# Kernel tuning notes

Hardware: AMD Instinct MI355X
Metric: run time of the kernel (lower is better)

## Reference

```python
import jax, jax.numpy as jnp
import numpy as np

N_NODE = 50000   # item vocab
D = 100          # embed_dim / hidden_size
N = 49152        # total nodes across all sessions
E = 98304        # edges
B = 4096         # sessions
STDV = 1.0 / np.sqrt(D)


def setup_inputs() -> dict:
    key = jax.random.key(0)
    ks = jax.random.split(key, 20)
    # 1-based item ids, shape [N,1] as in data.x
    x = jax.random.randint(ks[0], (N, 1), 1, N_NODE + 1, dtype=jnp.int32)
    edge_index = jax.random.randint(ks[1], (2, E), 0, N, dtype=jnp.int32)
    # sorted session ids; every session appears at least once (split/nodes[-1] needs non-empty)
    base = jnp.arange(B, dtype=jnp.int32)
    extra = jax.random.randint(ks[2], (N - B,), 0, B, dtype=jnp.int32)
    batch = jnp.sort(jnp.concatenate([base, extra]))

    def u(k, shape):
        return jax.random.uniform(k, shape, minval=-STDV, maxval=STDV, dtype=jnp.float32)

    return {
        "x": x, "edge_index": edge_index, "batch": batch, "num_sessions": B,
        "emb": u(ks[3], (N_NODE, D)),
        "conv_w": u(ks[4], (D, D)),          # GatedGraphConv weight[0]
        "gru_w_ih": u(ks[5], (3 * D, D)),
        "gru_w_hh": u(ks[6], (3 * D, D)),
        "gru_b_ih": u(ks[7], (3 * D,)),
        "gru_b_hh": u(ks[8], (3 * D,)),
        "q_w": u(ks[9], (1, D)), "q_b": u(ks[10], (1,)),
        "w2_w": u(ks[11], (D, D)), "w2_b": u(ks[12], (D,)),
        "w3_w": u(ks[13], (D, D)), "w3_b": u(ks[14], (D,)),
        "w4_w": u(ks[15], (D, 3 * D)), "w4_b": u(ks[16], (D,)),
    }


def _forward(x, edge_index, batch, num_sessions, emb, conv_w,
             gru_w_ih, gru_w_hh, gru_b_ih, gru_b_hh,
             q_w, q_b, w2_w, w2_b, w3_w, w3_b, w4_w, w4_b):
    ids = x[:, 0] - 1                              # data.x - 1
    h0 = emb[ids]                                  # [N, D]

    # GatedGraphConv(num_layers=1): m = x @ W; aggregate sum src->dst; GRUCell update
    src, dst = edge_index[0], edge_index[1]
    m = h0 @ conv_w                                # [N, D]
    agg = jnp.zeros_like(h0).at[dst].add(m[src])   # segment-sum aggregation
    gi = agg @ gru_w_ih.T + gru_b_ih               # [N, 3D]
    gh = h0 @ gru_w_hh.T + gru_b_hh
    i_r, i_z, i_n = jnp.split(gi, 3, axis=1)
    h_r, h_z, h_n = jnp.split(gh, 3, axis=1)
    r = jax.nn.sigmoid(i_r + h_r)
    z = jax.nn.sigmoid(i_z + h_z)
    n = jnp.tanh(i_n + r * h_n)
    xh = jax.nn.relu((1.0 - z) * n + z * h0)       # F.relu(Conv(x, edge_index))

    # last node per session (batch is sorted, sessions non-empty)
    counts = jax.ops.segment_sum(jnp.ones_like(batch), batch, num_segments=num_sessions)
    last_idx = jnp.cumsum(counts) - 1
    v_n = xh[last_idx]                             # [B, D]

    # get_scores: per-session softmax(v_n . nodes) weighted sum -> S_s
    logits = jnp.sum(xh * v_n[batch], axis=1)      # [N]
    mx = jax.ops.segment_max(logits, batch, num_segments=num_sessions)
    p = jnp.exp(logits - mx[batch])
    denom = jax.ops.segment_sum(p, batch, num_segments=num_sessions)
    score = p / denom[batch]                       # [N]
    S_s = jax.ops.segment_sum(score[:, None] * xh, batch, num_segments=num_sessions)

    # sigmoid-gated attention pooling -> S_g
    gate = jax.nn.sigmoid(xh @ w2_w.T + w2_b + v_n[batch] @ w3_w.T + w3_b)
    alpha = gate @ q_w.T + q_b                     # [N, 1]
    S_g = jax.ops.segment_sum(alpha * xh, batch, num_segments=num_sessions)

    S = jnp.concatenate([S_s, S_g, v_n], axis=1) @ w4_w.T + w4_b  # [B, D]
    y_hat = S @ emb.T                              # [B, n_node]
    return y_hat


def reference(x, edge_index, batch, num_sessions, emb, conv_w,
              gru_w_ih, gru_w_hh, gru_b_ih, gru_b_hh,
              q_w, q_b, w2_w, w2_b, w3_w, w3_b, w4_w, w4_b):
    return _forward(x, edge_index, batch, num_sessions, emb, conv_w,
                    gru_w_ih, gru_w_hh, gru_b_ih, gru_b_hh,
                    q_w, q_b, w2_w, w2_b, w3_w, w3_b, w4_w, w4_b)
```

## Files before the change

kernel.cpp:

```cpp
#include <hip/hip_runtime.h>
#include <math.h>

#define DDIM 100
#define PFD  4
#define NTG  4

using short8 = __attribute__((ext_vector_type(8))) short;
using f32x4  = __attribute__((ext_vector_type(4))) float;


__device__ __forceinline__ float sigm(float x) { return 1.f / (1.f + expf(-x)); }

__device__ __forceinline__ f32x4 mfma16(short8 a, short8 b, f32x4 c) {
  return __builtin_amdgcn_mfma_f32_16x16x32_bf16(a, b, c, 0, 0, 0);
}

__device__ __forceinline__ void gld_lds16(const void* g, void* l) {
  __builtin_amdgcn_global_load_lds(
      (const __attribute__((address_space(1))) void*)g,
      (__attribute__((address_space(3))) void*)l, 16, 0, 0);
}

__device__ __forceinline__ void bf16split(float v, short& h, short& l) {
  unsigned u = __float_as_uint(v);
  unsigned hb = (u + 0x7fffu + ((u >> 16) & 1u)) & 0xffff0000u;
  float res = v - __uint_as_float(hb);
  unsigned u2 = __float_as_uint(res);
  h = (short)(hb >> 16);
  l = (short)((u2 + 0x7fffu + ((u2 >> 16) & 1u)) >> 16);
}

__device__ __forceinline__ short bf16hi(float v) {
  unsigned u = __float_as_uint(v);
  return (short)((u + 0x7fffu + ((u >> 16) & 1u)) >> 16);
}

__global__ __launch_bounds__(256) void k_wc(const float* __restrict__ w_ih,
                                            const float* __restrict__ conv_w,
                                            float* __restrict__ Wc) {
  __shared__ float cwT[100 * 100];
  const int tid = threadIdx.x;
  for (int idx = tid; idx < 10000; idx += 256) {
    int k = idx / 100, t = idx - k * 100;
    cwT[t * 100 + k] = conv_w[idx];
  }
  __syncthreads();
  const int cBase = blockIdx.x * 25;
  for (int o = tid; o < 25 * 100; o += 256) {
    int c = cBase + o / 100;
    int k = o - (o / 100) * 100;
    const float* wr = w_ih + (size_t)c * 100;
    float acc = 0.f;
    for (int t = 0; t < 100; ++t) acc = fmaf(wr[t], cwT[t * 100 + k], acc);
    Wc[(size_t)c * 100 + k] = acc;
  }
}

__global__ void k_packAll(const int* __restrict__ batch, const float* __restrict__ emb,
                          const float* __restrict__ Wc,
                          const float* __restrict__ w_hh, const float* __restrict__ w2,
                          const float* __restrict__ w3,
                          short8* __restrict__ Bhi, short8* __restrict__ Blo,
                          short8* __restrict__ Whi, int* __restrict__ last_idx,
                          int NNODE, int NT, int N) {
  int gid = blockIdx.x * 256 + threadIdx.x;
  const int embN = NT * 4 * 64;
  const int wN = 8 * 7 * 4 * 64;
  if (gid < embN) {
    int lane = gid & 63;
    int kt = (gid >> 6) & 3;
    int rt = gid >> 8;
    int r = rt * 16 + (lane & 15);
    if (r >= NNODE) r = NNODE - 1;
    int k0 = kt * 32 + (lane >> 4) * 8;
    float4 f0 = make_float4(0.f, 0.f, 0.f, 0.f);
    float4 f1 = make_float4(0.f, 0.f, 0.f, 0.f);
    if (k0 < 100)     f0 = *(const float4*)(emb + (size_t)r * DDIM + k0);
    if (k0 + 4 < 100) f1 = *(const float4*)(emb + (size_t)r * DDIM + k0 + 4);
    float v[8] = {f0.x, f0.y, f0.z, f0.w, f1.x, f1.y, f1.z, f1.w};
    short8 h, l;
#pragma unroll
    for (int j = 0; j < 8; ++j) {
      short hh, ll;
      bf16split(v[j], hh, ll);
      h[j] = hh; l[j] = ll;
    }
    Bhi[gid] = h;
    Blo[gid] = l;
  } else if (gid < embN + wN) {
    int wg = gid - embN;
    int lane = wg & 63;
    int kt = (wg >> 6) & 3;
    int snt = wg >> 8;
    int nt = snt % 7;
    int s = snt / 7;
    int d = nt * 16 + (lane & 15);
    int k0 = kt * 32 + (lane >> 4) * 8;
    short8 h;
#pragma unroll
    for (int j = 0; j < 8; ++j) {
      int k = k0 + j;
      float v = 0.f;
      if (d < 100 && k < 100) {
        if (s < 3)      v = Wc[(size_t)(s * 100 + d) * 100 + k];
        else if (s < 6) v = w_hh[(size_t)((s - 3) * 100 + d) * 100 + k];
        else if (s == 6) v = w2[(size_t)d * 100 + k];
        else             v = w3[(size_t)d * 100 + k];
      }
      h[j] = bf16hi(v);
    }
    Whi[wg] = h;
  } else {
    int i = gid - embN - wN;
    if (i < N) {
      if (i == N - 1 || batch[i + 1] != batch[i]) last_idx[batch[i]] = i;
    }
  }
}

__global__ __launch_bounds__(512, 1) void k_aggGru(
    const int* __restrict__ ei, const int* __restrict__ x,
    const float* __restrict__ emb, const short8* __restrict__ Whi,
    const float* __restrict__ b_ih, const float* __restrict__ b_hh,
    const float* __restrict__ b2,
    float* __restrict__ xh, float* __restrict__ t2, int E) {
  __shared__ float acc[256 * DDIM];
  const int tid = threadIdx.x;
  const int lane = tid & 63;
  const int wave = tid >> 6;
  const int r0blk = blockIdx.x * 256;

  for (int idx = tid; idx < 256 * DDIM / 4; idx += 512)
    ((float4*)acc)[idx] = make_float4(0.f, 0.f, 0.f, 0.f);
  __syncthreads();

  const int per = E >> 3;
  const int base = wave * per;
  for (int it = 0; it < per; it += 256) {
    int e0 = base + it + lane * 4;
    int4 d4 = *(const int4*)(ei + E + e0);
    int4 s4 = *(const int4*)(ei + e0);
    int darr[4] = {d4.x, d4.y, d4.z, d4.w};
    int sarr[4] = {s4.x, s4.y, s4.z, s4.w};
#pragma unroll
    for (int j = 0; j < 4; ++j) {
      int dj = darr[j] - r0blk;
      bool match = (unsigned)dj < 256u;
      unsigned long long mask = __ballot(match);
      while (mask) {
        int bit = __ffsll(mask) - 1;
        mask &= mask - 1;
        int ds = __shfl(dj, bit, 64);
        int ss = __shfl(sarr[j], bit, 64);
        if (lane < 25) {
          int er = x[ss] - 1;
          float4 v = *(const float4*)(emb + (size_t)er * DDIM + 4 * lane);
          float* a = acc + ds * DDIM + 4 * lane;
          atomicAdd(a + 0, v.x); atomicAdd(a + 1, v.y);
          atomicAdd(a + 2, v.z); atomicAdd(a + 3, v.w);
        }
      }
    }
  }
  __syncthreads();

  const int lr = wave * 32;
  const int rowBase = r0blk + lr;
  const int c0 = lane & 15;
  const int rq = (lane >> 4) * 4;

  short8 aI0[4], aI1[4];
  {
    int r = lane & 15;
    int g = lane >> 4;
#pragma unroll
    for (int kt = 0; kt < 4; ++kt) {
      int k0 = kt * 32 + g * 8;
      short8 h0f, h1f;
#pragma unroll
      for (int j = 0; j < 8; ++j) {
        int k = k0 + j;
        float v0 = (k < 100) ? acc[(lr + r) * DDIM + k] : 0.f;
        float v1 = (k < 100) ? acc[(lr + 16 + r) * DDIM + k] : 0.f;
        h0f[j] = bf16hi(v0);
        h1f[j] = bf16hi(v1);
      }
      aI0[kt] = h0f;
      aI1[kt] = h1f;
    }
  }
  short8 aH0[4], aH1[4];
  {
    int r0g = x[rowBase + (lane & 15)] - 1;
    int r1g = x[rowBase + 16 + (lane & 15)] - 1;
    int g = lane >> 4;
#pragma unroll
    for (int kt = 0; kt < 4; ++kt) {
      int k0 = kt * 32 + g * 8;
      float4 a0f = make_float4(0.f, 0.f, 0.f, 0.f), a1f = a0f;
      float4 b0f = a0f, b1f = a0f;
      if (k0 < 100) {
        a0f = *(const float4*)(emb + (size_t)r0g * DDIM + k0);
        b0f = *(const float4*)(emb + (size_t)r1g * DDIM + k0);
      }
      if (k0 + 4 < 100) {
        a1f = *(const float4*)(emb + (size_t)r0g * DDIM + k0 + 4);
        b1f = *(const float4*)(emb + (size_t)r1g * DDIM + k0 + 4);
      }
      float v0[8] = {a0f.x, a0f.y, a0f.z, a0f.w, a1f.x, a1f.y, a1f.z, a1f.w};
      float v1[8] = {b0f.x, b0f.y, b0f.z, b0f.w, b1f.x, b1f.y, b1f.z, b1f.w};
      short8 h0f, h1f;
#pragma unroll
      for (int j = 0; j < 8; ++j) {
        h0f[j] = bf16hi(v0[j]);
        h1f[j] = bf16hi(v1[j]);
      }
      aH0[kt] = h0f;
      aH1[kt] = h1f;
    }
  }
  int xr0[4], xr1[4];
#pragma unroll
  for (int ri = 0; ri < 4; ++ri) {
    xr0[ri] = x[rowBase + rq + ri] - 1;
    xr1[ri] = x[rowBase + 16 + rq + ri] - 1;
  }

  for (int nt = 0; nt < 7; ++nt) {
    int d = nt * 16 + c0;
    f32x4 a0[6] = {};
    f32x4 a1[6] = {};
#pragma unroll
    for (int s = 0; s < 6; ++s) {
#pragma unroll
      for (int kt = 0; kt < 4; ++kt) {
        short8 w = Whi[(((size_t)s * 7 + nt) * 4 + kt) * 64 + lane];
        if (s < 3) {
          a0[s] = mfma16(aI0[kt], w, a0[s]);
          a1[s] = mfma16(aI1[kt], w, a1[s]);
        } else {
          a0[s] = mfma16(aH0[kt], w, a0[s]);
          a1[s] = mfma16(aH1[kt], w, a1[s]);
        }
      }
    }
    if (d < 100) {
      float bir = b_ih[d], biz = b_ih[100 + d], bin_ = b_ih[200 + d];
      float bhr = b_hh[d], bhz = b_hh[100 + d], bhn = b_hh[200 + d];
#pragma unroll
      for (int ri = 0; ri < 4; ++ri) {
        {
          float r = sigm(a0[0][ri] + bir + a0[3][ri] + bhr);
          float z = sigm(a0[1][ri] + biz + a0[4][ri] + bhz);
          float n = tanhf(a0[2][ri] + bin_ + r * (a0[5][ri] + bhn));
          float h0v = emb[(size_t)xr0[ri] * DDIM + d];
          float v = (1.f - z) * n + z * h0v;
          acc[(lr + rq + ri) * DDIM + d] = v > 0.f ? v : 0.f;
        }
        {
          float r = sigm(a1[0][ri] + bir + a1[3][ri] + bhr);
          float z = sigm(a1[1][ri] + biz + a1[4][ri] + bhz);
          float n = tanhf(a1[2][ri] + bin_ + r * (a1[5][ri] + bhn));
          float h0v = emb[(size_t)xr1[ri] * DDIM + d];
          float v = (1.f - z) * n + z * h0v;
          acc[(lr + 16 + rq + ri) * DDIM + d] = v > 0.f ? v : 0.f;
        }
      }
    }
  }

  const int dr = lane / 25;
  const int dc4 = (lane - dr * 25) * 4;
  if (lane < 50) {
#pragma unroll
    for (int p = 0; p < 16; ++p) {
      int row = p * 2 + dr;
      f32x4 v = *(const f32x4*)&acc[(lr + row) * DDIM + dc4];
      *(f32x4*)(xh + (size_t)(rowBase + row) * DDIM + dc4) = v;
    }
  }

  short8 xa0[4], xa1[4];
  {
    int r = lane & 15;
    int g = lane >> 4;
#pragma unroll
    for (int kt = 0; kt < 4; ++kt) {
      int k0 = kt * 32 + g * 8;
      short8 h0f, h1f;
#pragma unroll
      for (int j = 0; j < 8; ++j) {
        int k = k0 + j;
        float v0 = (k < 100) ? acc[(lr + r) * DDIM + k] : 0.f;
        float v1 = (k < 100) ? acc[(lr + 16 + r) * DDIM + k] : 0.f;
        h0f[j] = bf16hi(v0);
        h1f[j] = bf16hi(v1);
      }
      xa0[kt] = h0f;
      xa1[kt] = h1f;
    }
  }

  for (int nt = 0; nt < 7; ++nt) {
    int d = nt * 16 + c0;
    f32x4 ac0 = {0.f, 0.f, 0.f, 0.f};
    f32x4 ac1 = {0.f, 0.f, 0.f, 0.f};
#pragma unroll
    for (int kt = 0; kt < 4; ++kt) {
      short8 w = Whi[(((size_t)6 * 7 + nt) * 4 + kt) * 64 + lane];
      ac0 = mfma16(xa0[kt], w, ac0);
      ac1 = mfma16(xa1[kt], w, ac1);
    }
    if (d < 100) {
      float b = b2[d];
#pragma unroll
      for (int ri = 0; ri < 4; ++ri) {
        acc[(lr + rq + ri) * DDIM + d] = ac0[ri] + b;
        acc[(lr + 16 + rq + ri) * DDIM + d] = ac1[ri] + b;
      }
    }
  }
  if (lane < 50) {
#pragma unroll
    for (int p = 0; p < 16; ++p) {
      int row = p * 2 + dr;
      f32x4 v = *(const f32x4*)&acc[(lr + row) * DDIM + dc4];
      *(f32x4*)(t2 + (size_t)(rowBase + row) * DDIM + dc4) = v;
    }
  }
}

__global__ __launch_bounds__(256) void k_session(
    const float* __restrict__ xh, const float* __restrict__ t2,
    const float* __restrict__ t3v,
    const float* __restrict__ q_w, const float* __restrict__ q_b,
    const int* __restrict__ last_idx, float* __restrict__ Scat, int B) {
  int sid = blockIdx.x * 4 + (threadIdx.x >> 6);
  if (sid >= B) return;
  const int lane = threadIdx.x & 63;
  const int g = lane >> 4;
  const int s = lane & 15;
  const int start = (sid == 0) ? 0 : last_idx[sid - 1] + 1;
  const int end = last_idx[sid];

  float vr[7], t3r[7], qr[7];
#pragma unroll
  for (int k = 0; k < 7; ++k) {
    int c = s + 16 * k;
    bool ok = c < DDIM;
    vr[k]  = ok ? xh[(size_t)end * DDIM + c] : 0.f;
    t3r[k] = ok ? t3v[(size_t)sid * DDIM + c] : 0.f;
    qr[k]  = ok ? q_w[c] : 0.f;
  }
  const float qb = q_b[0];

  float m = -INFINITY, den = 0.f;
  float ss[7] = {}, sg[7] = {};
  for (int i = start; i <= end; i += 4) {
    int ni = i + g;
    bool act = ni <= end;
    int nrow = act ? ni : end;
    float xv[7];
    float l = 0.f, ga = 0.f;
#pragma unroll
    for (int k = 0; k < 7; ++k) {
      int c = s + 16 * k;
      float x = (c < DDIM) ? xh[(size_t)nrow * DDIM + c] : 0.f;
      float tv = (c < DDIM) ? t2[(size_t)nrow * DDIM + c] : 0.f;
      xv[k] = x;
      l = fmaf(x, vr[k], l);
      ga = fmaf(qr[k], sigm(tv + t3r[k]), ga);
    }
#pragma unroll
    for (int o = 1; o <= 8; o <<= 1) {
      l += __shfl_xor(l, o, 64);
      ga += __shfl_xor(ga, o, 64);
    }
    float ls = act ? l : -INFINITY;
    float alpha = act ? (ga + qb) : 0.f;
    float mn = fmaxf(m, ls);
    float cf = (m == -INFINITY) ? 0.f : expf(m - mn);
    float p = act ? expf(ls - mn) : 0.f;
    den = den * cf + p;
#pragma unroll
    for (int k = 0; k < 7; ++k) {
      ss[k] = ss[k] * cf + p * xv[k];
      sg[k] = fmaf(alpha, xv[k], sg[k]);
    }
    m = mn;
  }
  float mAll = m;
  mAll = fmaxf(mAll, __shfl_xor(mAll, 16, 64));
  mAll = fmaxf(mAll, __shfl_xor(mAll, 32, 64));
  float sc = (m == -INFINITY) ? 0.f : expf(m - mAll);
  float dv = den * sc;
  dv += __shfl_xor(dv, 16, 64);
  dv += __shfl_xor(dv, 32, 64);
  float inv = 1.f / dv;
  float* Sc = Scat + (size_t)sid * 300;
#pragma unroll
  for (int k = 0; k < 7; ++k) {
    float sv = ss[k] * sc;
    float gv = sg[k];
    sv += __shfl_xor(sv, 16, 64);  sv += __shfl_xor(sv, 32, 64);
    gv += __shfl_xor(gv, 16, 64);  gv += __shfl_xor(gv, 32, 64);
    int c = s + 16 * k;
    if (g == 0 && c < DDIM) {
      Sc[c] = sv * inv;
      Sc[100 + c] = gv;
      Sc[200 + c] = vr[k];
    }
  }
}

__device__ __forceinline__ void load_afragsHg(const float* __restrict__ A,
                                              const int* __restrict__ idx, int base,
                                              int lane, short8 ah[4]) {
  int r = idx[base + (lane & 15)];
  int g = lane >> 4;
#pragma unroll
  for (int kt = 0; kt < 4; ++kt) {
    int k0 = kt * 32 + g * 8;
    float4 f0 = make_float4(0.f, 0.f, 0.f, 0.f);
    float4 f1 = make_float4(0.f, 0.f, 0.f, 0.f);
    if (k0 < 100)     f0 = *(const float4*)(A + (size_t)r * DDIM + k0);
    if (k0 + 4 < 100) f1 = *(const float4*)(A + (size_t)r * DDIM + k0 + 4);
    short8 h;
    h[0] = bf16hi(f0.x); h[1] = bf16hi(f0.y); h[2] = bf16hi(f0.z); h[3] = bf16hi(f0.w);
    h[4] = bf16hi(f1.x); h[5] = bf16hi(f1.y); h[6] = bf16hi(f1.z); h[7] = bf16hi(f1.w);
    ah[kt] = h;
  }
}

__global__ __launch_bounds__(256) void k_t3v(
    const float* __restrict__ xh, const short8* __restrict__ Whi,
    const float* __restrict__ b3, const int* __restrict__ lastI,
    float* __restrict__ t3v) {
  const int lane = threadIdx.x & 63;
  const int wave = threadIdx.x >> 6;
  const int rowBase = blockIdx.x * 128 + wave * 32;
  short8 a0[4], a1[4];
  load_afragsHg(xh, lastI, rowBase, lane, a0);
  load_afragsHg(xh, lastI, rowBase + 16, lane, a1);
  const int c0 = lane & 15;
  const int r0 = (lane >> 4) * 4;

  for (int nt = 0; nt < 7; ++nt) {
    int d = nt * 16 + c0;
    f32x4 ac0 = {0.f, 0.f, 0.f, 0.f};
    f32x4 ac1 = {0.f, 0.f, 0.f, 0.f};
#pragma unroll
    for (int kt = 0; kt < 4; ++kt) {
      short8 w = Whi[(((size_t)7 * 7 + nt) * 4 + kt) * 64 + lane];
      ac0 = mfma16(a0[kt], w, ac0);
      ac1 = mfma16(a1[kt], w, ac1);
    }
    if (d < 100) {
      float b = b3[d];
#pragma unroll
      for (int ri = 0; ri < 4; ++ri) {
        t3v[(size_t)(rowBase + r0 + ri) * DDIM + d] = ac0[ri] + b;
        t3v[(size_t)(rowBase + 16 + r0 + ri) * DDIM + d] = ac1[ri] + b;
      }
    }
  }
}

__global__ __launch_bounds__(256, 2) void k_gemmS(
    const float* __restrict__ A, const float* __restrict__ Bm,
    const float* __restrict__ bias, short* __restrict__ Ph, short* __restrict__ Pl,
    int M) {
  __shared__ float4 As4[25 * 128];
  __shared__ float4 Bs4[25 * 64];
  const int m0 = blockIdx.y * 128;
  const int n0 = blockIdx.x * 64;
  const int t = threadIdx.x;
  const int tx = t & 15;
  const int ty = t >> 4;
  float acc[8][4] = {};

  for (int kt = 0; kt < 300; kt += 100) {
    for (int idx = t; idx < 128 * 25; idx += 256) {
      int r = idx / 25, k4 = idx - r * 25;
      int ar = m0 + r; if (ar >= M) ar = M - 1;
      float4 v = *(const float4*)(A + (size_t)ar * 300 + kt + 4 * k4);
      As4[k4 * 128 + (r ^ (k4 & 7))] = v;
    }
    for (int idx = t; idx < 64 * 25; idx += 256) {
      int r = idx / 25, k4 = idx - r * 25;
      int br = n0 + r;
      float4 v = make_float4(0.f, 0.f, 0.f, 0.f);
      if (br < 100) v = *(const float4*)(Bm + (size_t)br * 300 + kt + 4 * k4);
      Bs4[k4 * 64 + (r ^ (k4 & 7))] = v;
    }
    __syncthreads();
#pragma unroll 5
    for (int k4 = 0; k4 < 25; ++k4) {
      const int s = k4 & 7;
      float4 av[8], bv[4];
#pragma unroll
      for (int i = 0; i < 8; ++i) av[i] = As4[k4 * 128 + ((ty + 16 * i) ^ s)];
#pragma unroll
      for (int j = 0; j < 4; ++j) bv[j] = Bs4[k4 * 64 + ((tx + 16 * j) ^ s)];
#pragma unroll
      for (int i = 0; i < 8; ++i) {
#pragma unroll
        for (int j = 0; j < 4; ++j) {
          acc[i][j] = fmaf(av[i].x, bv[j].x, acc[i][j]);
          acc[i][j] = fmaf(av[i].y, bv[j].y, acc[i][j]);
          acc[i][j] = fmaf(av[i].z, bv[j].z, acc[i][j]);
          acc[i][j] = fmaf(av[i].w, bv[j].w, acc[i][j]);
        }
      }
    }
    __syncthreads();
  }

#pragma unroll
  for (int i = 0; i < 8; ++i) {
    int row = m0 + ty + 16 * i;
    if (row >= M) continue;
#pragma unroll
    for (int j = 0; j < 4; ++j) {
      int col = n0 + tx + 16 * j;
      float v = (col < 100) ? (acc[i][j] + bias[col]) : 0.f;
      short hh, ll;
      bf16split(v, hh, ll);
      int rt = row >> 4, kt = col >> 5;
      int lane_t = (row & 15) + 16 * ((col >> 3) & 3);
      size_t base = ((((size_t)rt * 4 + kt) * 64 + lane_t) << 3) + (col & 7);
      Ph[base] = hh;
      Pl[base] = ll;
    }
  }
}

__global__ __launch_bounds__(256) void k_bigmm(
    const short8* __restrict__ Ahi, const short8* __restrict__ Alo,
    const short8* __restrict__ Bhi, const short8* __restrict__ Blo,
    float* __restrict__ out, int NT, int NTCHUNK, int NCOLS) {
  __shared__ short8 Bs[PFD * 8 * 64];
  __shared__ float Xp[4 * 32 * 64];
  const int lane = threadIdx.x & 63;
  const int wave = threadIdx.x >> 6;
  const int mt0 = blockIdx.x * 8 + wave * 2;

  short8 ah[2][4], al[2][4];
#pragma unroll
  for (int mi = 0; mi < 2; ++mi)
#pragma unroll
    for (int kt = 0; kt < 4; ++kt) {
      size_t off = ((size_t)(mt0 + mi) * 4 + kt) * 64 + lane;
      ah[mi][kt] = Ahi[off];
      al[mi][kt] = Alo[off];
    }

  const int nt0 = blockIdx.y * NTCHUNK;
  const int nt1 = min(NT, nt0 + NTCHUNK);
  const int r0 = (lane >> 4) * 4;
  const int c0 = lane & 15;
  float* xp = &Xp[wave * 32 * 64];

  auto issueB = [&](int nt) {
    int s = nt & (PFD - 1);
    gld_lds16(Bhi + ((size_t)nt * 4 + wave) * 64 + lane, &Bs[(s * 8 + wave) * 64]);
    gld_lds16(Blo + ((size_t)nt * 4 + wave) * 64 + lane, &Bs[(s * 8 + 4 + wave) * 64]);
  };

  for (int i = 0; i < PFD && nt0 + i < nt1; ++i) issueB(nt0 + i);
  asm volatile("s_waitcnt vmcnt(6)" ::: "memory");
  __builtin_amdgcn_s_barrier();

  for (int g = nt0; g < nt1; g += NTG) {
    const int jn = min(NTG, nt1 - g);
    f32x4 acc[2][NTG] = {};
#pragma unroll
    for (int j = 0; j < NTG; ++j) {
      if (j >= jn) break;
      const int nt = g + j;
      const int s = nt & (PFD - 1);
      short8 bh[4], bl[4];
#pragma unroll
      for (int kt = 0; kt < 4; ++kt) {
        bh[kt] = Bs[(s * 8 + kt) * 64 + lane];
        bl[kt] = Bs[(s * 8 + 4 + kt) * 64 + lane];
      }
      asm volatile("s_waitcnt lgkmcnt(0)" ::: "memory");
      __builtin_amdgcn_s_barrier();
      if (nt + PFD < nt1) issueB(nt + PFD);
      __builtin_amdgcn_sched_barrier(0);
#pragma unroll
      for (int kt = 0; kt < 4; ++kt) {
        acc[0][j] = mfma16(ah[0][kt], bh[kt], acc[0][j]);
        acc[1][j] = mfma16(ah[1][kt], bh[kt], acc[1][j]);
        acc[0][j] = mfma16(ah[0][kt], bl[kt], acc[0][j]);
        acc[1][j] = mfma16(ah[1][kt], bl[kt], acc[1][j]);
        acc[0][j] = mfma16(al[0][kt], bh[kt], acc[0][j]);
        acc[1][j] = mfma16(al[1][kt], bh[kt], acc[1][j]);
      }
      asm volatile("s_waitcnt vmcnt(14)" ::: "memory");
      __builtin_amdgcn_s_barrier();
    }
#pragma unroll
    for (int mi = 0; mi < 2; ++mi)
#pragma unroll
      for (int j = 0; j < NTG; ++j) {
        if (j < jn) {
#pragma unroll
          for (int r = 0; r < 4; ++r) {
            int rl = mi * 16 + r0 + r;
            int cl = j * 16 + c0;
            xp[rl * 64 + (cl ^ (((rl >> 2) & 3) << 4))] = acc[mi][j][r];
          }
        }
      }
    const int colbase = g * 16;
#pragma unroll
    for (int it = 0; it < 8; ++it) {
      int rl = it * 4 + (lane >> 4);
      int cl = 4 * c0;
      if (cl < jn * 16) {
        f32x4 v = *(const f32x4*)&xp[rl * 64 + (cl ^ (((rl >> 2) & 3) << 4))];
        int row = mt0 * 16 + rl;
        __builtin_nontemporal_store(v, (f32x4*)(out + (size_t)row * NCOLS + colbase + cl));
      }
    }
  }
}


extern "C" void kernel_launch(void* const* d_in, const int* in_sizes, int n_in,
                              void* d_out, int out_size, void* d_ws, size_t ws_size,
                              hipStream_t stream) {
  const int*   x      = (const int*)d_in[0];
  const int*   ei     = (const int*)d_in[1];
  const int*   batch  = (const int*)d_in[2];
  const float* emb    = (const float*)d_in[4];
  const float* conv_w = (const float*)d_in[5];
  const float* w_ih   = (const float*)d_in[6];
  const float* w_hh   = (const float*)d_in[7];
  const float* b_ih   = (const float*)d_in[8];
  const float* b_hh   = (const float*)d_in[9];
  const float* q_w    = (const float*)d_in[10];
  const float* q_b    = (const float*)d_in[11];
  const float* w2     = (const float*)d_in[12];
  const float* b2     = (const float*)d_in[13];
  const float* w3     = (const float*)d_in[14];
  const float* b3     = (const float*)d_in[15];
  const float* w4     = (const float*)d_in[16];
  const float* b4     = (const float*)d_in[17];

  const int N = in_sizes[0];
  const int E = in_sizes[1] / 2;
  const int NNODE = in_sizes[4] / DDIM;
  const int B = out_size / NNODE;

  size_t ND = (size_t)N * DDIM;
  float* ws   = (float*)d_ws;
  float* xh   = ws;
  float* t2   = ws + ND;
  float* aux  = ws + 2 * ND;
  float* t3v  = aux;
  float* Scat = t3v + (size_t)B * DDIM;
  int*   lastI = (int*)(Scat + 3 * (size_t)B * DDIM);

  const int MT = (B + 15) / 16;
  const int NT = (NNODE + 15) / 16;
  short8* Whi = (short8*)(lastI + B);
  short8* Ahi = Whi + 8 * 7 * 4 * 64;
  short8* Alo = Ahi + (size_t)MT * 4 * 64;
  short8* Bhi = Alo + (size_t)MT * 4 * 64;
  short8* Blo = Bhi + (size_t)NT * 4 * 64;
  float*  Wc  = (float*)(Blo + (size_t)NT * 4 * 64);

  dim3 blk(256);
  const int nblkB = B / 128;

  int packTotal = NT * 4 * 64 + 8 * 7 * 4 * 64 + N;
  k_wc<<<12, blk, 0, stream>>>(w_ih, conv_w, Wc);
  k_packAll<<<(packTotal + 255) / 256, blk, 0, stream>>>(
      batch, emb, Wc, w_hh, w2, w3, Bhi, Blo, Whi, lastI, NNODE, NT, N);
  k_aggGru<<<N / 256, dim3(512), 0, stream>>>(ei, x, emb, Whi, b_ih, b_hh, b2,
                                              xh, t2, E);
  k_t3v<<<nblkB, blk, 0, stream>>>(xh, Whi, b3, lastI, t3v);
  k_session<<<(B + 3) / 4, blk, 0, stream>>>(xh, t2, t3v, q_w, q_b, lastI, Scat, B);
  k_gemmS<<<dim3(2, B / 128), blk, 0, stream>>>(Scat, w4, b4, (short*)Ahi, (short*)Alo, B);

  const int NTCHUNK = 48;
  const int NCHUNKS = (NT + NTCHUNK - 1) / NTCHUNK;
  k_bigmm<<<dim3(nblkB, NCHUNKS), blk, 0, stream>>>(
      Ahi, Alo, Bhi, Blo, (float*)d_out, NT, NTCHUNK, NNODE);
}
```

Baseline: 394.2 us.

## Compact matching edges into LDS queue before per-thread row accumulation

Edge-scatter aggregation no longer uses a per-match ballot/shuffle loop where only 25 lanes of a wave gather one embedding row at a time. Each thread now tests its edges, looks up the source item id, and appends a packed (dst,row) entry to a shared-memory queue. After a barrier, each thread gathers one full 100-float row and accumulates it with LDS atomics, which removes the serialized wave loop and idle lanes. In exchange, each thread reads a full row (uncoalesced across lanes), and any overflow past 1024 entries falls back to a slow per-thread path.

```diff
diff --git a/kernel.cpp b/kernel.cpp
--- a/kernel.cpp
+++ b/kernel.cpp
@@ -4,6 +4,7 @@
 #define DDIM 100
 #define PFD  4
 #define NTG  4
+#define QMAX 1024
 
 using short8 = __attribute__((ext_vector_type(8))) short;
 using f32x4  = __attribute__((ext_vector_type(4))) float;
@@ -125,19 +126,21 @@
     const float* __restrict__ b2,
     float* __restrict__ xh, float* __restrict__ t2, int E) {
   __shared__ float acc[256 * DDIM];
+  __shared__ int qpack[QMAX];
+  __shared__ int qc;
   const int tid = threadIdx.x;
   const int lane = tid & 63;
   const int wave = tid >> 6;
   const int r0blk = blockIdx.x * 256;
 
+  if (tid == 0) qc = 0;
   for (int idx = tid; idx < 256 * DDIM / 4; idx += 512)
     ((float4*)acc)[idx] = make_float4(0.f, 0.f, 0.f, 0.f);
   __syncthreads();
 
-  const int per = E >> 3;
-  const int base = wave * per;
-  for (int it = 0; it < per; it += 256) {
-    int e0 = base + it + lane * 4;
+  const int nIter = E / (512 * 4);
+  for (int c = 0; c < nIter; ++c) {
+    int e0 = (c * 512 + tid) * 4;
     int4 d4 = *(const int4*)(ei + E + e0);
     int4 s4 = *(const int4*)(ei + e0);
     int darr[4] = {d4.x, d4.y, d4.z, d4.w};
@@ -145,21 +148,37 @@
 #pragma unroll
     for (int j = 0; j < 4; ++j) {
       int dj = darr[j] - r0blk;
-      bool match = (unsigned)dj < 256u;
-      unsigned long long mask = __ballot(match);
-      while (mask) {
-        int bit = __ffsll(mask) - 1;
-        mask &= mask - 1;
-        int ds = __shfl(dj, bit, 64);
-        int ss = __shfl(sarr[j], bit, 64);
-        if (lane < 25) {
-          int er = x[ss] - 1;
-          float4 v = *(const float4*)(emb + (size_t)er * DDIM + 4 * lane);
-          float* a = acc + ds * DDIM + 4 * lane;
-          atomicAdd(a + 0, v.x); atomicAdd(a + 1, v.y);
-          atomicAdd(a + 2, v.z); atomicAdd(a + 3, v.w);
+      if ((unsigned)dj < 256u) {
+        int er = x[sarr[j]] - 1;
+        int pos = atomicAdd(&qc, 1);
+        if (pos < QMAX) {
+          qpack[pos] = (dj << 16) | er;
+        } else {
+          const float* src = emb + (size_t)er * DDIM;
+          float* a = acc + dj * DDIM;
+          for (int cc = 0; cc < 25; ++cc) {
+            float4 v = *(const float4*)(src + 4 * cc);
+            atomicAdd(a + 4 * cc + 0, v.x); atomicAdd(a + 4 * cc + 1, v.y);
+            atomicAdd(a + 4 * cc + 2, v.z); atomicAdd(a + 4 * cc + 3, v.w);
+          }
         }
       }
+    }
+  }
+  __syncthreads();
+
+  const int Q = qc < QMAX ? qc : QMAX;
+  for (int q = tid; q < Q; q += 512) {
+    int pk = qpack[q];
+    int dj = pk >> 16;
+    int er = pk & 0xffff;
+    const float* src = emb + (size_t)er * DDIM;
+    float* a = acc + dj * DDIM;
+#pragma unroll
+    for (int cc = 0; cc < 25; ++cc) {
+      float4 v = *(const float4*)(src + 4 * cc);
+      atomicAdd(a + 4 * cc + 0, v.x); atomicAdd(a + 4 * cc + 1, v.y);
+      atomicAdd(a + 4 * cc + 2, v.z); atomicAdd(a + 4 * cc + 3, v.w);
     }
   }
   __syncthreads();
@@ -193,10 +212,9 @@
   {
     int r0g = x[rowBase + (lane & 15)] - 1;
     int r1g = x[rowBase + 16 + (lane & 15)] - 1;
-    int g = lane >> 4;
 #pragma unroll
     for (int kt = 0; kt < 4; ++kt) {
-      int k0 = kt * 32 + g * 8;
+      int k0 = kt * 32 + (lane >> 4) * 8;
       float4 a0f = make_float4(0.f, 0.f, 0.f, 0.f), a1f = a0f;
       float4 b0f = a0f, b1f = a0f;
       if (k0 < 100) {
```

Result: no change. 396.6 us (+0.6%).
